# Performance work log

Hardware: AMD Instinct MI355X
Metric: run time of the kernel (lower is better)

The kernel has to match this reference:

```python
import jax, jax.numpy as jnp
import numpy as np

B, S, D, H = 4, 2048, 512, 4
HD = D // H
EPS = 1e-5


def layer_norm(x, gamma, beta):
    mu = jnp.mean(x, axis=-1, keepdims=True)
    var = jnp.mean(jnp.square(x - mu), axis=-1, keepdims=True)
    return (x - mu) * jax.lax.rsqrt(var + EPS) * gamma + beta


def setup_inputs() -> dict:
    key = jax.random.key(0)
    ks = jax.random.split(key, 16)
    s_in = 1.0 / np.sqrt(D)
    s_ex = 1.0 / np.sqrt(2 * D)
    return {
        "input_states": jax.random.normal(ks[0], (B, S, D), jnp.float32),
        "positions": jax.random.normal(ks[1], (B, S, 3), jnp.float32),
        "W_expand": jax.random.uniform(ks[2], (D, 2 * D), jnp.float32, -s_in, s_in),
        "b_expand": jax.random.uniform(ks[3], (2 * D,), jnp.float32, -s_in, s_in),
        "W_squeeze": jax.random.uniform(ks[4], (2 * D, D), jnp.float32, -s_ex, s_ex),
        "b_squeeze": jax.random.uniform(ks[5], (D,), jnp.float32, -s_ex, s_ex),
        "gamma": jnp.ones((D,), jnp.float32),
        "beta": jnp.zeros((D,), jnp.float32),
        "Wq": jax.random.uniform(ks[6], (D, D), jnp.float32, -s_in, s_in),
        "bq": jax.random.uniform(ks[7], (D,), jnp.float32, -s_in, s_in),
        "Wk": jax.random.uniform(ks[8], (D, D), jnp.float32, -s_in, s_in),
        "bk": jax.random.uniform(ks[9], (D,), jnp.float32, -s_in, s_in),
        "Wv": jax.random.uniform(ks[10], (D, D), jnp.float32, -s_in, s_in),
        "bv": jax.random.uniform(ks[11], (D,), jnp.float32, -s_in, s_in),
        "alpha": jnp.float32(0.1),
    }


def reference(input_states, positions, W_expand, b_expand, W_squeeze, b_squeeze,
              gamma, beta, Wq, bq, Wk, bk, Wv, bv, alpha):
    # FFN (expand -> relu -> squeeze) + residual + LayerNorm
    h = jax.nn.relu(input_states @ W_expand + b_expand)
    squeezed = h @ W_squeeze + b_squeeze
    se = layer_norm(input_states + squeezed, gamma, beta)

    # q/k/v projections, split heads: [B,H,S,HD]
    q = (se @ Wq + bq).reshape(B, S, H, HD).transpose(0, 2, 1, 3)
    k = (se @ Wk + bk).reshape(B, S, H, HD).transpose(0, 2, 1, 3)
    v = (se @ Wv + bv).reshape(B, S, H, HD).transpose(0, 2, 1, 3)

    scores = jnp.einsum('bhid,bhjd->bhij', q, k) / np.sqrt(HD)

    # squared pairwise distance bias: ||pi||^2 + ||pj||^2 - 2 pi.pj, broadcast over heads
    sq = jnp.sum(positions * positions, axis=-1)  # [B,S]
    dist2 = sq[:, :, None] + sq[:, None, :] - 2.0 * jnp.einsum('bic,bjc->bij', positions, positions)
    dist2 = jnp.maximum(dist2, 0.0)
    scores = scores - alpha * dist2[:, None, :, :]

    w = jax.nn.softmax(scores, axis=-1)
    ctx = jnp.einsum('bhij,bhjd->bhid', w, v)
    ctx = ctx.transpose(0, 2, 1, 3).reshape(B, S, D)

    # same LayerNorm params reused (self.norm applied twice in original)
    return layer_norm(se + ctx, gamma, beta)
```

## Files before the change

### kernel.cpp

```cpp
#include <hip/hip_runtime.h>

typedef __bf16 bf16_t;
typedef __attribute__((ext_vector_type(8))) __bf16 bf16x8;
typedef __attribute__((ext_vector_type(4))) __bf16 bf16x4;
typedef __attribute__((ext_vector_type(4))) float f32x4;
typedef __attribute__((ext_vector_type(16))) float f32x16;

constexpr int Bc = 4, Sc = 2048, Dc = 512, Hc = 4, HDc = 128;
constexpr int Mrows = Bc * Sc;

__device__ inline void gl2lds(const void* g, void* l) {
  __builtin_amdgcn_global_load_lds(
      (__attribute__((address_space(1))) void*)g,
      (__attribute__((address_space(3))) void*)l, 16, 0, 0);
}

__global__ __launch_bounds__(256) void prep_k(
    const float* __restrict__ X, bf16_t* __restrict__ xb,
    const float* __restrict__ pos, const float* __restrict__ alphap,
    bf16_t* __restrict__ Qbg, bf16_t* __restrict__ Kbg,
    const float* __restrict__ We, bf16_t* __restrict__ wtE,
    const float* __restrict__ Ws, bf16_t* __restrict__ wtS,
    const float* __restrict__ Wq, const float* __restrict__ Wk,
    const float* __restrict__ Wv, bf16_t* __restrict__ wtQKV) {
  const int bid = blockIdx.x;
  if (bid < 2048) {
    const long i = ((long)bid * 256 + threadIdx.x) * 8;
    const float4 a = *(const float4*)(X + i);
    const float4 c = *(const float4*)(X + i + 4);
    bf16x8 o;
    o[0] = (bf16_t)a.x; o[1] = (bf16_t)a.y; o[2] = (bf16_t)a.z; o[3] = (bf16_t)a.w;
    o[4] = (bf16_t)c.x; o[5] = (bf16_t)c.y; o[6] = (bf16_t)c.z; o[7] = (bf16_t)c.w;
    *(bf16x8*)(xb + i) = o;
    return;
  }
  if (bid < 2080) {
    const float ap = alphap[0] * 11.313708498984761f;
    const int i = (bid - 2048) * 256 + threadIdx.x;
    const int b = i >> 11, s = i & 2047;
    const float x = pos[(long)i * 3], y = pos[(long)i * 3 + 1], z = pos[(long)i * 3 + 2];
    const float m2 = -ap * (x * x + y * y + z * z);
    bf16x8 qlo = {}, klo = {}, zer = {};
    qlo[0] = (bf16_t)(2.f * ap * x); qlo[1] = (bf16_t)(2.f * ap * y);
    qlo[2] = (bf16_t)(2.f * ap * z); qlo[3] = (bf16_t)1.0f;
    klo[0] = (bf16_t)x; klo[1] = (bf16_t)y; klo[2] = (bf16_t)z; klo[3] = (bf16_t)m2;
    *(bf16x8*)(Qbg + (long)i * 16) = qlo;
    *(bf16x8*)(Qbg + (long)i * 16 + 8) = zer;
    const int t = s >> 6, kh = (s >> 5) & 1, key = s & 31;
    const long kb = ((long)(b * 32 + t) * 2 + kh) * 512 + key * 8;
    *(bf16x8*)(Kbg + kb) = klo;
    *(bf16x8*)(Kbg + kb + 256) = zer;
    return;
  }
  __shared__ float tile[32][33];
  const float* src; bf16_t* dst; int K, N, local;
  if (bid < 2592)      { src = We; dst = wtE; K = 512;  N = 1024; local = bid - 2080; }
  else if (bid < 3104) { src = Ws; dst = wtS; K = 1024; N = 512;  local = bid - 2592; }
  else if (bid < 3360) { src = Wq; dst = wtQKV;          K = 512; N = 512; local = bid - 3104; }
  else if (bid < 3616) { src = Wk; dst = wtQKV + 262144; K = 512; N = 512; local = bid - 3360; }
  else                 { src = Wv; dst = wtQKV + 524288; K = 512; N = 512; local = bid - 3616; }
  const int nb = N / 32;
  const int n0 = (local % nb) * 32, k0 = (local / nb) * 32;
  const int tx = threadIdx.x & 31, ty = threadIdx.x >> 5;
#pragma unroll
  for (int i = 0; i < 4; i++)
    tile[ty + i * 8][tx] = src[(long)(k0 + ty + i * 8) * N + n0 + tx];
  __syncthreads();
#pragma unroll
  for (int i = 0; i < 4; i++)
    dst[(long)(n0 + ty + i * 8) * K + k0 + tx] = (bf16_t)tile[tx][ty + i * 8];
}

template <int OMODE, int TN, int NB>
__global__ __launch_bounds__(256, (TN == 128) ? 2 : 3) void gemm128_k(
    const bf16_t* __restrict__ A, const bf16_t* __restrict__ Bt,
    const float* __restrict__ bias0, const float* __restrict__ bias1,
    const float* __restrict__ bias2, void* __restrict__ out0,
    void* __restrict__ out1, void* __restrict__ out2, int N, int K) {
  __shared__ bf16_t As[2][128 * 64];
  __shared__ bf16_t Bs[2][TN * 64];
  constexpr int MT = (TN == 128) ? 4 : 2;
  constexpr int BI = (TN == 128) ? 4 : 2;
  constexpr int MW = (TN == 128) ? 64 : 32;
  const int t = threadIdx.x;
  const int p = blockIdx.x;
  const int slot = p >> 3;
  const int by = (p & 7) + 8 * (slot / NB);
  const int bx = slot % NB;
  const int n0 = bx * TN, m0 = by * 128;
  const int lane = t & 63, wave = t >> 6;
  const int quad = lane >> 4, ln = lane & 15;
  const int wm = (TN == 128) ? (wave >> 1) : wave;
  const int wn = (TN == 128) ? (wave & 1) : 0;
  const int l8 = lane >> 3, g = lane & 7;
  const bf16_t* aseg = A + (long)(m0 + wave * 32 + l8) * K + (g ^ l8) * 8;
  const bf16_t* bseg = Bt + (long)(n0 + wave * (BI * 8) + l8) * K + (g ^ l8) * 8;
  auto stage = [&](int buf, int k0) {
#pragma unroll
    for (int i = 0; i < 4; i++)
      gl2lds(aseg + (long)i * 8 * K + k0, &As[buf][(wave * 32 + i * 8) * 64]);
#pragma unroll
    for (int i = 0; i < BI; i++)
      gl2lds(bseg + (long)i * 8 * K + k0, &Bs[buf][(wave * BI * 8 + i * 8) * 64]);
  };
  f32x4 acc[MT][4] = {};
  stage(0, 0);
  const int niter = K / 64;
  for (int it = 0; it < niter; it++) {
    const int cur = it & 1;
    __syncthreads();
    if (it + 1 < niter) stage(1 - cur, (it + 1) * 64);
#pragma unroll
    for (int kc = 0; kc < 2; kc++) {
      bf16x8 af[MT], bfr[4];
#pragma unroll
      for (int mt = 0; mt < MT; mt++)
        af[mt] = *(const bf16x8*)&As[cur][(wm * MW + mt * 16 + ln) * 64 +
                                          (((kc * 4 + quad) ^ (ln & 7)) * 8)];
#pragma unroll
      for (int nt = 0; nt < 4; nt++)
        bfr[nt] = *(const bf16x8*)&Bs[cur][(wn * 64 + nt * 16 + ln) * 64 +
                                           (((kc * 4 + quad) ^ (ln & 7)) * 8)];
#pragma unroll
      for (int mt = 0; mt < MT; mt++)
#pragma unroll
        for (int nt = 0; nt < 4; nt++)
          acc[mt][nt] = __builtin_amdgcn_mfma_f32_16x16x32_bf16(af[mt], bfr[nt],
                                                                acc[mt][nt], 0, 0, 0);
    }
  }
#pragma unroll
  for (int nt = 0; nt < 4; nt++) {
    const int gcol = n0 + wn * 64 + nt * 16 + ln;
    if constexpr (OMODE == 0 || OMODE == 1) {
      const float bv = bias0[gcol];
      bf16_t* o = (bf16_t*)out0;
#pragma unroll
      for (int mt = 0; mt < MT; mt++)
#pragma unroll
        for (int r = 0; r < 4; r++) {
          const int grow = m0 + wm * MW + mt * 16 + quad * 4 + r;
          float vv = acc[mt][nt][r] + bv;
          if constexpr (OMODE == 0) vv = vv > 0.f ? vv : 0.f;
          o[(long)grow * N + gcol] = (bf16_t)vv;
        }
    } else {
      const int which = gcol >> 9, n = gcol & 511;
      const int hh = n >> 7, hd = n & 127;
      const float bv = (which == 0 ? bias0 : which == 1 ? bias1 : bias2)[n];
      bf16_t* o = (bf16_t*)(which == 0 ? out0 : which == 1 ? out1 : out2);
#pragma unroll
      for (int mt = 0; mt < MT; mt++)
#pragma unroll
        for (int r = 0; r < 4; r++) {
          const int grow = m0 + wm * MW + mt * 16 + quad * 4 + r;
          const int b = grow >> 11, s = grow & 2047;
          const float vv = acc[mt][nt][r] + bv;
          long idx;
          if (which == 0) {
            idx = ((long)((b * Hc + hh) * Sc + s)) * HDc + hd;
          } else if (which == 1) {
            const int tt = s >> 6, kh = (s >> 5) & 1, key = s & 31;
            const int c = hd >> 4, lk = key + 32 * ((hd >> 3) & 1), j = hd & 7;
            idx = ((((long)((b * Hc + hh) * 32 + tt) * 2 + kh) * 8 + c) * 64 + lk) * 8 + j;
          } else {
            const int tt = s >> 6, ht2 = hd >> 5, kc = (s & 63) >> 4;
            const int lk = (hd & 31) + 32 * ((s >> 3) & 1), j = s & 7;
            idx = ((((long)((b * Hc + hh) * 32 + tt) * 4 + ht2) * 4 + kc) * 64 + lk) * 8 + j;
          }
          o[idx] = (bf16_t)vv;
        }
    }
  }
}

template <int AF32, int OF32>
__global__ __launch_bounds__(256) void ln_k(const void* __restrict__ xa,
                                            const bf16_t* __restrict__ xb,
                                            const float* __restrict__ gamma,
                                            const float* __restrict__ beta,
                                            void* __restrict__ out) {
  const int wave = threadIdx.x >> 6, lane = threadIdx.x & 63;
  const long row = (long)blockIdx.x * 4 + wave;
  const int col0 = lane * 8;
  float vv[8];
  float s = 0.f, s2 = 0.f;
  const bf16x8 vb = *(const bf16x8*)(xb + row * Dc + col0);
  if constexpr (AF32) {
    const float* a = (const float*)xa + row * Dc + col0;
    const float4 a0 = *(const float4*)a;
    const float4 a1 = *(const float4*)(a + 4);
    const float xs[8] = {a0.x, a0.y, a0.z, a0.w, a1.x, a1.y, a1.z, a1.w};
#pragma unroll
    for (int j = 0; j < 8; j++) vv[j] = xs[j] + (float)vb[j];
  } else {
    const bf16x8 va = *(const bf16x8*)((const bf16_t*)xa + row * Dc + col0);
#pragma unroll
    for (int j = 0; j < 8; j++) vv[j] = (float)va[j] + (float)vb[j];
  }
#pragma unroll
  for (int j = 0; j < 8; j++) { s += vv[j]; s2 += vv[j] * vv[j]; }
#pragma unroll
  for (int off = 1; off < 64; off <<= 1) {
    s += __shfl_xor(s, off, 64);
    s2 += __shfl_xor(s2, off, 64);
  }
  const float mu = s * (1.f / Dc);
  const float var = s2 * (1.f / Dc) - mu * mu;
  const float rstd = rsqrtf(var + 1e-5f);
  const float4 g0 = *(const float4*)(gamma + col0);
  const float4 g1 = *(const float4*)(gamma + col0 + 4);
  const float4 b0 = *(const float4*)(beta + col0);
  const float4 b1 = *(const float4*)(beta + col0 + 4);
  const float gs[8] = {g0.x, g0.y, g0.z, g0.w, g1.x, g1.y, g1.z, g1.w};
  const float bs[8] = {b0.x, b0.y, b0.z, b0.w, b1.x, b1.y, b1.z, b1.w};
  if constexpr (OF32) {
    float* o = (float*)out + row * Dc + col0;
    float4 o0, o1;
    o0.x = (vv[0] - mu) * rstd * gs[0] + bs[0];
    o0.y = (vv[1] - mu) * rstd * gs[1] + bs[1];
    o0.z = (vv[2] - mu) * rstd * gs[2] + bs[2];
    o0.w = (vv[3] - mu) * rstd * gs[3] + bs[3];
    o1.x = (vv[4] - mu) * rstd * gs[4] + bs[4];
    o1.y = (vv[5] - mu) * rstd * gs[5] + bs[5];
    o1.z = (vv[6] - mu) * rstd * gs[6] + bs[6];
    o1.w = (vv[7] - mu) * rstd * gs[7] + bs[7];
    *(float4*)o = o0; *(float4*)(o + 4) = o1;
  } else {
    bf16x8 ob;
#pragma unroll
    for (int j = 0; j < 8; j++) ob[j] = (bf16_t)((vv[j] - mu) * rstd * gs[j] + bs[j]);
    *(bf16x8*)((bf16_t*)out + row * Dc + col0) = ob;
  }
}

__global__ __launch_bounds__(256, 2) void attn_k(const bf16_t* __restrict__ q,
                                                 const bf16_t* __restrict__ Kg,
                                                 const bf16_t* __restrict__ Vg,
                                                 const bf16_t* __restrict__ Qbg,
                                                 const bf16_t* __restrict__ Kbg,
                                                 bf16_t* __restrict__ ctx) {
  __shared__ bf16_t Ks[2][8192];
  __shared__ bf16_t Vts[2][8192];
  __shared__ bf16_t Kb[2][1024];
  __shared__ bf16_t Ps[4][1024];
  __shared__ float RsD[4][32];
  const int t = threadIdx.x;
  const int p = blockIdx.x;
  const int qt = (p >> 3) & 31;
  const int gg = (p & 7) + 8 * (p >> 8);
  const int h = gg & 3, b = gg >> 2;
  const int q0 = qt * 64;
  const int wave = t >> 6, lane = t & 63;
  const int l31 = lane & 31, hb = lane >> 5;
  const int rh = wave & 1, kh = wave >> 1;
  const float scale_l2 = 1.4426950408889634f * 0.08838834764831845f;

  bf16x8 qf[8], qbf;
  const long qrow = (long)((b * Hc + h) * Sc + q0 + rh * 32 + l31);
#pragma unroll
  for (int c = 0; c < 8; c++)
    qf[c] = *(const bf16x8*)(q + qrow * HDc + c * 16 + hb * 8);
  qbf = *(const bf16x8*)(Qbg + (long)(b * Sc + q0 + rh * 32 + l31) * 16 + hb * 8);

  const bf16_t* ktile = Kg + (long)((b * Hc + h) * 32) * 8192 + lane * 8;
  const bf16_t* vtile = Vg + (long)((b * Hc + h) * 32) * 8192 + lane * 8;
  const bf16_t* kbtile = Kbg + (long)(b * 32) * 1024 + lane * 8;
  auto stage = [&](int buf) {
#pragma unroll
    for (int i = 0; i < 4; i++)
      gl2lds(ktile + (wave * 4 + i) * 512, &Ks[buf][(wave * 4 + i) * 512]);
#pragma unroll
    for (int i = 0; i < 4; i++)
      gl2lds(vtile + (wave * 4 + i) * 512, &Vts[buf][(wave * 4 + i) * 512]);
    if (wave < 2) gl2lds(kbtile + wave * 512, &Kb[buf][wave * 512]);
  };
  stage(0);
  ktile += 8192; vtile += 8192; kbtile += 1024;

  float rsl = 0.f;
  f32x16 accT[4] = {};
  bf16_t* pwbase = &Ps[wave][l31 * 8 + 4 * hb];

  for (int kt = 0; kt < Sc / 64; kt++) {
    const int cur = kt & 1;
    __syncthreads();
    if (kt < Sc / 64 - 1) {
      stage(1 - cur);
      ktile += 8192; vtile += 8192; kbtile += 1024;
    }
    f32x16 sa = {}, sb = {};
#pragma unroll
    for (int c = 0; c < 4; c++) {
      const bf16x8 kf = *(const bf16x8*)&Ks[cur][(kh * 8 + c) * 512 + lane * 8];
      sa = __builtin_amdgcn_mfma_f32_32x32x16_bf16(kf, qf[c], sa, 0, 0, 0);
    }
#pragma unroll
    for (int c = 4; c < 8; c++) {
      const bf16x8 kf = *(const bf16x8*)&Ks[cur][(kh * 8 + c) * 512 + lane * 8];
      sb = __builtin_amdgcn_mfma_f32_32x32x16_bf16(kf, qf[c], sb, 0, 0, 0);
    }
    {
      const bf16x8 kbf = *(const bf16x8*)&Kb[cur][kh * 512 + lane * 8];
      sb = __builtin_amdgcn_mfma_f32_32x32x16_bf16(kbf, qbf, sb, 0, 0, 0);
    }
    const f32x16 sacc = sa + sb;
#pragma unroll
    for (int g2 = 0; g2 < 4; g2++) {
      bf16x4 pq4;
#pragma unroll
      for (int r0 = 0; r0 < 4; r0++) {
        const float pe = __builtin_amdgcn_exp2f(sacc[g2 * 4 + r0] * scale_l2);
        rsl += pe;
        pq4[r0] = (bf16_t)pe;
      }
      *(bf16x4*)(pwbase + (g2 >> 1) * 512 + (g2 & 1) * 256) = pq4;
    }
    const bf16x8 pf0 = *(const bf16x8*)&Ps[wave][lane * 8];
    const bf16x8 pf1 = *(const bf16x8*)&Ps[wave][512 + lane * 8];
#pragma unroll
    for (int ht = 0; ht < 4; ht++) {
      const bf16x8 v0 = *(const bf16x8*)&Vts[cur][(ht * 4 + kh * 2 + 0) * 512 + lane * 8];
      accT[ht] = __builtin_amdgcn_mfma_f32_32x32x16_bf16(v0, pf0, accT[ht], 0, 0, 0);
      const bf16x8 v1 = *(const bf16x8*)&Vts[cur][(ht * 4 + kh * 2 + 1) * 512 + lane * 8];
      accT[ht] = __builtin_amdgcn_mfma_f32_32x32x16_bf16(v1, pf1, accT[ht], 0, 0, 0);
    }
  }
  __syncthreads();

  rsl += __shfl_xor(rsl, 32, 64);
  if (hb == 0) RsD[wave][l31] = rsl;
  float* Oc = (float*)&Ks[0][0];
  if (kh == 1) {
#pragma unroll
    for (int ht = 0; ht < 4; ht++)
#pragma unroll
      for (int r = 0; r < 16; r++) {
        const int hdp = (r & 3) + 8 * (r >> 2) + 4 * hb;
        Oc[(ht * 32 + hdp) * 64 + rh * 32 + l31] = accT[ht][r];
      }
  }
  __syncthreads();
  if (kh == 0) {
    const float rinv = 1.f / (RsD[wave][l31] + RsD[wave + 2][l31]);
    const long orow = (long)(b * Sc + q0 + rh * 32 + l31);
#pragma unroll
    for (int ht = 0; ht < 4; ht++)
#pragma unroll
      for (int g2 = 0; g2 < 4; g2++) {
        bf16x4 ov;
#pragma unroll
        for (int r0 = 0; r0 < 4; r0++) {
          const int hdp = r0 + 8 * g2 + 4 * hb;
          ov[r0] = (bf16_t)((accT[ht][g2 * 4 + r0] +
                             Oc[(ht * 32 + hdp) * 64 + rh * 32 + l31]) * rinv);
        }
        *(bf16x4*)(ctx + orow * Dc + h * HDc + ht * 32 + 8 * g2 + 4 * hb) = ov;
      }
  }
}

constexpr size_t SQB_OFF = 0;
constexpr size_t SEB_OFF = 8388608;
constexpr size_t Q_OFF = 16777216;
constexpr size_t K_OFF = 25165824;
constexpr size_t V_OFF = 33554432;
constexpr size_t XB_OFF = Q_OFF;
constexpr size_t H_OFF = K_OFF;
constexpr size_t QBG_OFF = 41943040;
constexpr size_t KBG_OFF = QBG_OFF + 262144;
constexpr size_t WTE_OFF = KBG_OFF + 262144;
constexpr size_t WTS_OFF = WTE_OFF + 1048576;
constexpr size_t WTQKV_OFF = WTS_OFF + 1048576;

extern "C" void kernel_launch(void* const* d_in, const int* in_sizes, int n_in,
                              void* d_out, int out_size, void* d_ws, size_t ws_size,
                              hipStream_t stream) {
  const float* X = (const float*)d_in[0];
  const float* pos = (const float*)d_in[1];
  const float* W_expand = (const float*)d_in[2];
  const float* b_expand = (const float*)d_in[3];
  const float* W_squeeze = (const float*)d_in[4];
  const float* b_squeeze = (const float*)d_in[5];
  const float* gamma = (const float*)d_in[6];
  const float* beta = (const float*)d_in[7];
  const float* Wq = (const float*)d_in[8];
  const float* bq = (const float*)d_in[9];
  const float* Wk = (const float*)d_in[10];
  const float* bk = (const float*)d_in[11];
  const float* Wv = (const float*)d_in[12];
  const float* bv = (const float*)d_in[13];
  const float* alphap = (const float*)d_in[14];

  char* ws = (char*)d_ws;
  bf16_t* sqb = (bf16_t*)(ws + SQB_OFF);
  bf16_t* ctxb = (bf16_t*)(ws + SQB_OFF);
  bf16_t* seb = (bf16_t*)(ws + SEB_OFF);
  bf16_t* qbg = (bf16_t*)(ws + QBG_OFF);
  bf16_t* kbg = (bf16_t*)(ws + KBG_OFF);
  bf16_t* qb = (bf16_t*)(ws + Q_OFF);
  bf16_t* kb = (bf16_t*)(ws + K_OFF);
  bf16_t* vb = (bf16_t*)(ws + V_OFF);
  bf16_t* xbb = (bf16_t*)(ws + XB_OFF);
  bf16_t* hb = (bf16_t*)(ws + H_OFF);
  bf16_t* wtE = (bf16_t*)(ws + WTE_OFF);
  bf16_t* wtS = (bf16_t*)(ws + WTS_OFF);
  bf16_t* wtQKV = (bf16_t*)(ws + WTQKV_OFF);

  prep_k<<<3872, 256, 0, stream>>>(X, xbb, pos, alphap, qbg, kbg,
                                   W_expand, wtE, W_squeeze, wtS, Wq, Wk, Wv, wtQKV);
  gemm128_k<0, 128, 8><<<512, 256, 0, stream>>>(
      xbb, wtE, b_expand, nullptr, nullptr, hb, nullptr, nullptr, 1024, 512);
  gemm128_k<1, 64, 8><<<512, 256, 0, stream>>>(
      hb, wtS, b_squeeze, nullptr, nullptr, sqb, nullptr, nullptr, 512, 1024);
  ln_k<1, 0><<<Mrows / 4, 256, 0, stream>>>(X, sqb, gamma, beta, seb);
  gemm128_k<2, 128, 12><<<768, 256, 0, stream>>>(
      seb, wtQKV, bq, bk, bv, qb, kb, vb, 1536, 512);
  attn_k<<<512, 256, 0, stream>>>(qb, kb, vb, qbg, kbg, ctxb);
  ln_k<0, 1><<<Mrows / 4, 256, 0, stream>>>(seb, ctxb, gamma, beta, (float*)d_out);

  (void)in_sizes; (void)n_in; (void)out_size; (void)ws_size;
}
```

Measured before the change: 215.6 us.

## Load V and key bias directly from global, exchange P via lane shuffles

V tiles and the key-bias fragments are no longer staged through LDS. Each wave now reads them straight from global memory inside the loop. The softmax probabilities are packed into registers and swapped between half-waves with shuffles, which removes the LDS round trip for P. s_setprio raises wave priority around the MFMA sections. Together these cut LDS traffic and LDS footprint, which may allow more occupancy, but the global loads for V now sit on the critical path without double buffering and may add latency.

```diff
diff --git a/kernel.cpp b/kernel.cpp
--- a/kernel.cpp
+++ b/kernel.cpp
@@ -241,9 +241,6 @@
                                                  const bf16_t* __restrict__ Kbg,
                                                  bf16_t* __restrict__ ctx) {
   __shared__ bf16_t Ks[2][8192];
-  __shared__ bf16_t Vts[2][8192];
-  __shared__ bf16_t Kb[2][1024];
-  __shared__ bf16_t Ps[4][1024];
   __shared__ float RsD[4][32];
   const int t = threadIdx.x;
   const int p = blockIdx.x;
@@ -264,32 +261,29 @@
   qbf = *(const bf16x8*)(Qbg + (long)(b * Sc + q0 + rh * 32 + l31) * 16 + hb * 8);
 
   const bf16_t* ktile = Kg + (long)((b * Hc + h) * 32) * 8192 + lane * 8;
-  const bf16_t* vtile = Vg + (long)((b * Hc + h) * 32) * 8192 + lane * 8;
-  const bf16_t* kbtile = Kbg + (long)(b * 32) * 1024 + lane * 8;
+  const bf16_t* vbase = Vg + (long)((b * Hc + h) * 32) * 8192 + kh * 1024 + lane * 8;
+  const bf16_t* kbbase = Kbg + (long)(b * 32) * 1024 + kh * 512 + lane * 8;
   auto stage = [&](int buf) {
 #pragma unroll
     for (int i = 0; i < 4; i++)
       gl2lds(ktile + (wave * 4 + i) * 512, &Ks[buf][(wave * 4 + i) * 512]);
-#pragma unroll
-    for (int i = 0; i < 4; i++)
-      gl2lds(vtile + (wave * 4 + i) * 512, &Vts[buf][(wave * 4 + i) * 512]);
-    if (wave < 2) gl2lds(kbtile + wave * 512, &Kb[buf][wave * 512]);
   };
   stage(0);
-  ktile += 8192; vtile += 8192; kbtile += 1024;
+  ktile += 8192;
 
   float rsl = 0.f;
   f32x16 accT[4] = {};
-  bf16_t* pwbase = &Ps[wave][l31 * 8 + 4 * hb];
 
   for (int kt = 0; kt < Sc / 64; kt++) {
     const int cur = kt & 1;
     __syncthreads();
     if (kt < Sc / 64 - 1) {
       stage(1 - cur);
-      ktile += 8192; vtile += 8192; kbtile += 1024;
-    }
+      ktile += 8192;
+    }
+    const bf16x8 kbf = *(const bf16x8*)(kbbase + (long)kt * 1024);
     f32x16 sa = {}, sb = {};
+    __builtin_amdgcn_s_setprio(1);
 #pragma unroll
     for (int c = 0; c < 4; c++) {
       const bf16x8 kf = *(const bf16x8*)&Ks[cur][(kh * 8 + c) * 512 + lane * 8];
@@ -300,31 +294,47 @@
       const bf16x8 kf = *(const bf16x8*)&Ks[cur][(kh * 8 + c) * 512 + lane * 8];
       sb = __builtin_amdgcn_mfma_f32_32x32x16_bf16(kf, qf[c], sb, 0, 0, 0);
     }
-    {
-      const bf16x8 kbf = *(const bf16x8*)&Kb[cur][kh * 512 + lane * 8];
-      sb = __builtin_amdgcn_mfma_f32_32x32x16_bf16(kbf, qbf, sb, 0, 0, 0);
-    }
+    sb = __builtin_amdgcn_mfma_f32_32x32x16_bf16(kbf, qbf, sb, 0, 0, 0);
+    __builtin_amdgcn_s_setprio(0);
     const f32x16 sacc = sa + sb;
-#pragma unroll
-    for (int g2 = 0; g2 < 4; g2++) {
-      bf16x4 pq4;
-#pragma unroll
-      for (int r0 = 0; r0 < 4; r0++) {
-        const float pe = __builtin_amdgcn_exp2f(sacc[g2 * 4 + r0] * scale_l2);
-        rsl += pe;
-        pq4[r0] = (bf16_t)pe;
-      }
-      *(bf16x4*)(pwbase + (g2 >> 1) * 512 + (g2 & 1) * 256) = pq4;
-    }
-    const bf16x8 pf0 = *(const bf16x8*)&Ps[wave][lane * 8];
-    const bf16x8 pf1 = *(const bf16x8*)&Ps[wave][512 + lane * 8];
+
+    float pe[16];
+#pragma unroll
+    for (int i = 0; i < 16; i++) {
+      pe[i] = __builtin_amdgcn_exp2f(sacc[i] * scale_l2);
+      rsl += pe[i];
+    }
+    auto pk = [](float lo, float hi) -> int {
+      const unsigned short a = __builtin_bit_cast(unsigned short, (bf16_t)lo);
+      const unsigned short c = __builtin_bit_cast(unsigned short, (bf16_t)hi);
+      return (int)((unsigned)a | ((unsigned)c << 16));
+    };
+    const int W0 = pk(pe[0], pe[1]), W1 = pk(pe[2], pe[3]);
+    const int W2 = pk(pe[4], pe[5]), W3 = pk(pe[6], pe[7]);
+    const int W4 = pk(pe[8], pe[9]), W5 = pk(pe[10], pe[11]);
+    const int W6 = pk(pe[12], pe[13]), W7 = pk(pe[14], pe[15]);
+    const int X0 = __shfl_xor(W0, 32, 64), X1 = __shfl_xor(W1, 32, 64);
+    const int X2 = __shfl_xor(W2, 32, 64), X3 = __shfl_xor(W3, 32, 64);
+    const int X4 = __shfl_xor(W4, 32, 64), X5 = __shfl_xor(W5, 32, 64);
+    const int X6 = __shfl_xor(W6, 32, 64), X7 = __shfl_xor(W7, 32, 64);
+    union PF { int w[4]; bf16x8 v; };
+    PF u0, u1;
+    u0.w[0] = hb ? X2 : W0; u0.w[1] = hb ? X3 : W1;
+    u0.w[2] = hb ? W2 : X0; u0.w[3] = hb ? W3 : X1;
+    u1.w[0] = hb ? X6 : W4; u1.w[1] = hb ? X7 : W5;
+    u1.w[2] = hb ? W6 : X4; u1.w[3] = hb ? W7 : X5;
+    const bf16x8 pf0 = u0.v, pf1 = u1.v;
+
+    const bf16_t* vt = vbase + (long)kt * 8192;
+    __builtin_amdgcn_s_setprio(1);
 #pragma unroll
     for (int ht = 0; ht < 4; ht++) {
-      const bf16x8 v0 = *(const bf16x8*)&Vts[cur][(ht * 4 + kh * 2 + 0) * 512 + lane * 8];
+      const bf16x8 v0 = *(const bf16x8*)(vt + ht * 2048);
       accT[ht] = __builtin_amdgcn_mfma_f32_32x32x16_bf16(v0, pf0, accT[ht], 0, 0, 0);
-      const bf16x8 v1 = *(const bf16x8*)&Vts[cur][(ht * 4 + kh * 2 + 1) * 512 + lane * 8];
+      const bf16x8 v1 = *(const bf16x8*)(vt + ht * 2048 + 512);
       accT[ht] = __builtin_amdgcn_mfma_f32_32x32x16_bf16(v1, pf1, accT[ht], 0, 0, 0);
     }
+    __builtin_amdgcn_s_setprio(0);
   }
   __syncthreads();
 
```

New measurement: 276.2 us. 28.1% more time.

## Keep softmax probabilities in registers by permuting V layout; add MFMA priority hints

Applied to the files above, without the earlier changes.

The V tile is stored with the key index within each 16-key chunk permuted, so the S accumulator's register order directly matches the B-operand layout of the PV MFMA. This removes the per-iteration LDS write and read of the probability tile (and the Ps buffer). It also wraps the MFMA sections in s_setprio to favour matrix issue across waves. The cost is a more intricate V store pattern in the projection kernel, and correctness depends on the permutation matching the MFMA lane mapping exactly.

```diff
diff --git a/kernel.cpp b/kernel.cpp
--- a/kernel.cpp
+++ b/kernel.cpp
@@ -164,9 +164,11 @@
             const int c = hd >> 4, lk = key + 32 * ((hd >> 3) & 1), j = hd & 7;
             idx = ((((long)((b * Hc + hh) * 32 + tt) * 2 + kh) * 8 + c) * 64 + lk) * 8 + j;
           } else {
-            const int tt = s >> 6, ht2 = hd >> 5, kc = (s & 63) >> 4;
-            const int lk = (hd & 31) + 32 * ((s >> 3) & 1), j = s & 7;
-            idx = ((((long)((b * Hc + hh) * 32 + tt) * 4 + ht2) * 4 + kc) * 64 + lk) * 8 + j;
+            const int tt = s >> 6, ht2 = hd >> 5, kc2 = (s & 63) >> 4;
+            const int kl = s & 15;
+            const int klp = (kl & 3) | ((kl & 4) << 1) | ((kl & 8) >> 1);
+            const int lk = (hd & 31) + 32 * (klp >> 3), j = klp & 7;
+            idx = ((((long)((b * Hc + hh) * 32 + tt) * 4 + ht2) * 4 + kc2) * 64 + lk) * 8 + j;
           }
           o[idx] = (bf16_t)vv;
         }
@@ -243,7 +245,6 @@
   __shared__ bf16_t Ks[2][8192];
   __shared__ bf16_t Vts[2][8192];
   __shared__ bf16_t Kb[2][1024];
-  __shared__ bf16_t Ps[4][1024];
   __shared__ float RsD[4][32];
   const int t = threadIdx.x;
   const int p = blockIdx.x;
@@ -280,7 +281,6 @@
 
   float rsl = 0.f;
   f32x16 accT[4] = {};
-  bf16_t* pwbase = &Ps[wave][l31 * 8 + 4 * hb];
 
   for (int kt = 0; kt < Sc / 64; kt++) {
     const int cur = kt & 1;
@@ -290,6 +290,7 @@
       ktile += 8192; vtile += 8192; kbtile += 1024;
     }
     f32x16 sa = {}, sb = {};
+    __builtin_amdgcn_s_setprio(1);
 #pragma unroll
     for (int c = 0; c < 4; c++) {
       const bf16x8 kf = *(const bf16x8*)&Ks[cur][(kh * 8 + c) * 512 + lane * 8];
@@ -304,20 +305,23 @@
       const bf16x8 kbf = *(const bf16x8*)&Kb[cur][kh * 512 + lane * 8];
       sb = __builtin_amdgcn_mfma_f32_32x32x16_bf16(kbf, qbf, sb, 0, 0, 0);
     }
+    __builtin_amdgcn_s_setprio(0);
     const f32x16 sacc = sa + sb;
-#pragma unroll
-    for (int g2 = 0; g2 < 4; g2++) {
-      bf16x4 pq4;
-#pragma unroll
-      for (int r0 = 0; r0 < 4; r0++) {
-        const float pe = __builtin_amdgcn_exp2f(sacc[g2 * 4 + r0] * scale_l2);
-        rsl += pe;
-        pq4[r0] = (bf16_t)pe;
-      }
-      *(bf16x4*)(pwbase + (g2 >> 1) * 512 + (g2 & 1) * 256) = pq4;
-    }
-    const bf16x8 pf0 = *(const bf16x8*)&Ps[wave][lane * 8];
-    const bf16x8 pf1 = *(const bf16x8*)&Ps[wave][512 + lane * 8];
+
+    float pe[16];
+#pragma unroll
+    for (int i = 0; i < 16; i++) {
+      pe[i] = __builtin_amdgcn_exp2f(sacc[i] * scale_l2);
+      rsl += pe[i];
+    }
+    bf16x8 pf0, pf1;
+#pragma unroll
+    for (int j = 0; j < 8; j++) {
+      pf0[j] = (bf16_t)pe[j];
+      pf1[j] = (bf16_t)pe[8 + j];
+    }
+
+    __builtin_amdgcn_s_setprio(1);
 #pragma unroll
     for (int ht = 0; ht < 4; ht++) {
       const bf16x8 v0 = *(const bf16x8*)&Vts[cur][(ht * 4 + kh * 2 + 0) * 512 + lane * 8];
@@ -325,6 +329,7 @@
       const bf16x8 v1 = *(const bf16x8*)&Vts[cur][(ht * 4 + kh * 2 + 1) * 512 + lane * 8];
       accT[ht] = __builtin_amdgcn_mfma_f32_32x32x16_bf16(v1, pf1, accT[ht], 0, 0, 0);
     }
+    __builtin_amdgcn_s_setprio(0);
   }
   __syncthreads();
 
```

Result: no change. 214.5 us (-0.5%).
